# Optimization experiments

Hardware: AMD Instinct MI355X
Metric: run time of the kernel (lower is better)

Reference implementation:

```python
import jax, jax.numpy as jnp
import numpy as np

B, L, D = 2, 2048, 2048
H, HD = 16, 128
E = 8192
SCALE = float(np.sqrt(HD))


def setup_inputs() -> dict:
    key = jax.random.key(0)
    ks = jax.random.split(key, 8)
    s = 0.02
    x = jax.random.normal(ks[0], (B, L, D), dtype=jnp.float32)
    # causal mask: True where key position j > query position i (masked out)
    mask = jnp.triu(jnp.ones((L, L), dtype=bool), k=1)
    Wq = jax.random.normal(ks[1], (D, D), dtype=jnp.float32) * s
    Wk = jax.random.normal(ks[2], (D, D), dtype=jnp.float32) * s
    Wv = jax.random.normal(ks[3], (D, D), dtype=jnp.float32) * s
    W1 = jax.random.normal(ks[4], (D, E), dtype=jnp.float32) * s
    Vg = jax.random.normal(ks[5], (D, E), dtype=jnp.float32) * s
    W2 = jax.random.normal(ks[6], (E, D), dtype=jnp.float32) * s
    return {"x": x, "mask": mask, "Wq": Wq, "Wk": Wk, "Wv": Wv,
            "W1": W1, "Vg": Vg, "W2": W2}


def reynolds_fn(s):
    # Reynolds (group-averaging) operator over key axis: blend score with its row mean
    return 0.5 * s + 0.5 * jnp.mean(s, axis=-1, keepdims=True)


def reference(x, mask, Wq, Wk, Wv, W1, Vg, W2):
    b, l, d = x.shape
    q = (x @ Wq).reshape(b, l, H, HD).transpose(0, 2, 1, 3)  # (B,H,L,hd)
    k = (x @ Wk).reshape(b, l, H, HD).transpose(0, 2, 1, 3)
    v = (x @ Wv).reshape(b, l, H, HD).transpose(0, 2, 1, 3)
    scores = jnp.einsum('bhqd,bhkd->bhqk', q, k) / SCALE
    scores = reynolds_fn(scores)
    scores = jnp.where(mask[None, None], -jnp.inf, scores)
    attn = jax.nn.softmax(scores, axis=-1)
    out = jnp.einsum('bhqk,bhkd->bhqd', attn, v)
    out = out.transpose(0, 2, 1, 3).reshape(b, l, d)  # (B,L,D)
    h = jax.nn.silu(out @ W1) * (out @ Vg)  # SwiGLU
    return h @ W2
```

## Files before the change

kernel.cpp:

```cpp
#include <hip/hip_runtime.h>
#include <stdint.h>

typedef unsigned short u16;
typedef __attribute__((ext_vector_type(8))) short bf16x8;
typedef __attribute__((ext_vector_type(4))) float f32x4;

#define DEVINL static __device__ __forceinline__

DEVINL void gload_lds16(const void* g, void* l) {
  __builtin_amdgcn_global_load_lds(
      (const __attribute__((address_space(1))) unsigned int*)g,
      (__attribute__((address_space(3))) unsigned int*)l, 16, 0, 0);
}

DEVINL u16 f2b(float f) {
  union { float f; unsigned u; } v; v.f = f;
  unsigned r = (v.u + 0x7FFFu + ((v.u >> 16) & 1u)) >> 16;
  return (u16)r;
}

DEVINL bf16x8 ldsv8(const u16* p) { return *(const bf16x8*)p; }

__global__ __launch_bounds__(256) void convt_f32_bf16(
    const float* __restrict__ in, u16* __restrict__ out, int R, int C) {
  __shared__ u16 t[64][65];
  const int c0 = blockIdx.x * 64, r0 = blockIdx.y * 64;
  const int tx = threadIdx.x & 63, ty = threadIdx.x >> 6;
#pragma unroll
  for (int i = 0; i < 64; i += 4)
    t[ty + i][tx] = f2b(in[(size_t)(r0 + ty + i) * C + c0 + tx]);
  __syncthreads();
#pragma unroll
  for (int i = 0; i < 64; i += 4)
    out[(size_t)(c0 + ty + i) * R + r0 + tx] = t[tx][ty + i];
}

__global__ __launch_bounds__(256) void conv_f32_bf16(
    const float* __restrict__ in, u16* __restrict__ out) {
  const size_t i = ((size_t)blockIdx.x * 256 + threadIdx.x) * 4;
  const float4 v = *(const float4*)(in + i);
  ushort4 o;
  o.x = f2b(v.x); o.y = f2b(v.y); o.z = f2b(v.z); o.w = f2b(v.w);
  *(ushort4*)(out + i) = o;
}

template <int EPI>
__global__ __launch_bounds__(256, 2) void gemm_bt(
    const u16* __restrict__ A, const u16* __restrict__ B1,
    const u16* __restrict__ B2, u16* __restrict__ C, float* __restrict__ Cf,
    u16* __restrict__ Ck, u16* __restrict__ Cv,
    int M, int N, int K) {
  constexpr int BK = 64;
  __shared__ __align__(16) u16 sA[128 * BK];
  __shared__ __align__(16) u16 sB[128 * BK];
  __shared__ __align__(16) u16 sB2[(EPI == 2) ? 128 * BK : 16];

  const int tid = threadIdx.x;
  const int w = tid >> 6, lane = tid & 63;
  const int ln = lane & 15, quad = lane >> 4;
  const int wm = (w >> 1) << 6;
  const int wn = (w & 1) << 6;
  const size_t m0 = (size_t)blockIdx.y * 128;
  const size_t n0 = (size_t)blockIdx.x * 128;
  const int srow = lane >> 3;
  const int scol = (((lane & 7) ^ (lane >> 3)) << 3);

  const f32x4 z4 = {0.f, 0.f, 0.f, 0.f};
  f32x4 acc[4][4];
  f32x4 acc2[(EPI == 2) ? 4 : 1][(EPI == 2) ? 4 : 1];
#pragma unroll
  for (int i = 0; i < 4; ++i)
#pragma unroll
    for (int j = 0; j < 4; ++j) {
      acc[i][j] = z4;
      if constexpr (EPI == 2) acc2[i][j] = z4;
    }

  const int nkt = K >> 6;
  for (int kt = 0; kt < nkt; ++kt) {
    const int k0 = kt << 6;
    __syncthreads();
#pragma unroll
    for (int i = 0; i < 4; ++i) {
      const int j = (w << 2) + i;
      const int row = (j << 3) + srow;
      gload_lds16(A + (m0 + row) * K + (k0 + scol), &sA[j * 512]);
      gload_lds16(B1 + (n0 + row) * K + (k0 + scol), &sB[j * 512]);
      if constexpr (EPI == 2)
        gload_lds16(B2 + (n0 + row) * K + (k0 + scol), &sB2[j * 512]);
    }
    __syncthreads();
#pragma unroll
    for (int kk = 0; kk < 2; ++kk) {
      const int xc = (((kk << 2) + quad) ^ (ln & 7)) << 3;
      bf16x8 a[4];
#pragma unroll
      for (int mi = 0; mi < 4; ++mi)
        a[mi] = ldsv8(&sA[(wm + mi * 16 + ln) * BK + xc]);
#pragma unroll
      for (int ni = 0; ni < 4; ++ni) {
        bf16x8 b = ldsv8(&sB[(wn + ni * 16 + ln) * BK + xc]);
#pragma unroll
        for (int mi = 0; mi < 4; ++mi)
          acc[mi][ni] =
              __builtin_amdgcn_mfma_f32_16x16x32_bf16(a[mi], b, acc[mi][ni], 0, 0, 0);
      }
      if constexpr (EPI == 2) {
#pragma unroll
        for (int ni = 0; ni < 4; ++ni) {
          bf16x8 b = ldsv8(&sB2[(wn + ni * 16 + ln) * BK + xc]);
#pragma unroll
          for (int mi = 0; mi < 4; ++mi)
            acc2[mi][ni] =
                __builtin_amdgcn_mfma_f32_16x16x32_bf16(a[mi], b, acc2[mi][ni], 0, 0, 0);
        }
      }
    }
  }

#pragma unroll
  for (int mi = 0; mi < 4; ++mi)
#pragma unroll
    for (int ni = 0; ni < 4; ++ni)
#pragma unroll
      for (int r = 0; r < 4; ++r) {
        const size_t rg = m0 + wm + mi * 16 + quad * 4 + r;
        const size_t cg = n0 + wn + ni * 16 + ln;
        const float v = acc[mi][ni][r];
        if constexpr (EPI == 0) {
          Cf[rg * N + cg] = v;
        } else if constexpr (EPI == 4) {
          const size_t b = rg >> 11, l = rg & 2047;
          const size_t c = cg & 2047, h = c >> 7, hd = c & 127;
          const int which = (int)(cg >> 11);
          if (which == 0)
            C[(((b << 4) + h) * 2048 + l) * 128 + hd] = f2b(v);
          else if (which == 1)
            Ck[(((b << 4) + h) * 2048 + l) * 128 + hd] = f2b(v);
          else
            Cv[(((b << 4) + h) * 128 + hd) * 2048 + l] = f2b(v);
        } else {
          const float v2 = acc2[mi][ni][r];
          const float s = v / (1.f + __expf(-v));
          C[rg * N + cg] = f2b(s * v2);
        }
      }
}

__global__ __launch_bounds__(256, 2) void attn(
    const u16* __restrict__ Q, const u16* __restrict__ Km,
    const u16* __restrict__ VT, u16* __restrict__ O) {
  constexpr int L = 2048, HD = 128, QT = 128, KT = 64;
  __shared__ __align__(16) u16 sQ[QT * HD];
  __shared__ __align__(16) u16 sKP[QT * KT];
  __shared__ __align__(16) u16 sV[HD * KT];

  const int bh = blockIdx.y;
  const int q0 = blockIdx.x * QT;
  const int tid = threadIdx.x, w = tid >> 6, lane = tid & 63;
  const int ln = lane & 15, quad = lane >> 4;
  const int wr = w * 32;

  const u16* Qb = Q + (size_t)bh * L * HD + (size_t)q0 * HD;
  const u16* Kb = Km + (size_t)bh * L * HD;
  const u16* Vb = VT + (size_t)bh * HD * L;

#pragma unroll
  for (int i = 0; i < 8; ++i) {
    const int j = w * 8 + i;
    const int row = j * 4 + (lane >> 4);
    const int c = (lane & 15) ^ (row & 15);
    gload_lds16(Qb + row * HD + c * 8, &sQ[j * 512]);
  }

  const f32x4 z4 = {0.f, 0.f, 0.f, 0.f};
  float l_st[2][4];
  f32x4 accO[2][8];
#pragma unroll
  for (int mi = 0; mi < 2; ++mi) {
#pragma unroll
    for (int r = 0; r < 4; ++r) l_st[mi][r] = 0.f;
#pragma unroll
    for (int nt = 0; nt < 8; ++nt) accO[mi][nt] = z4;
  }

  const float scale = 0.04419417382415922f;
  const int nkt = (q0 >> 6) + 2;

  for (int kt = 0; kt < nkt; ++kt) {
    const int kb = kt << 6;
    __syncthreads();
#pragma unroll
    for (int i = 0; i < 4; ++i) {
      const int j = (w << 2) + i;
      const int krow = j * 4 + (lane >> 4);
      const int kc = (lane & 15) ^ (krow & 15);
      gload_lds16(Kb + (size_t)(kb + krow) * HD + kc * 8, &sKP[j * 512]);
      const int vrow = (j << 3) + (lane >> 3);
      const int vc = (lane & 7) ^ (lane >> 3);
      gload_lds16(Vb + (size_t)vrow * L + kb + vc * 8, &sV[j * 512]);
    }
    __syncthreads();

    f32x4 accS[2][4];
#pragma unroll
    for (int mi = 0; mi < 2; ++mi)
#pragma unroll
      for (int ct = 0; ct < 4; ++ct) accS[mi][ct] = z4;
#pragma unroll
    for (int kk = 0; kk < 4; ++kk) {
      const int xc = (((kk << 2) + quad) ^ ln) << 3;
      bf16x8 aq[2];
#pragma unroll
      for (int mi = 0; mi < 2; ++mi)
        aq[mi] = ldsv8(&sQ[(wr + mi * 16 + ln) * HD + xc]);
#pragma unroll
      for (int ct = 0; ct < 4; ++ct) {
        bf16x8 bk = ldsv8(&sKP[(ct * 16 + ln) * HD + xc]);
#pragma unroll
        for (int mi = 0; mi < 2; ++mi)
          accS[mi][ct] =
              __builtin_amdgcn_mfma_f32_16x16x32_bf16(aq[mi], bk, accS[mi][ct], 0, 0, 0);
      }
    }
    __syncthreads();

    const bool maskt = (kb + KT > q0);
#pragma unroll
    for (int mi = 0; mi < 2; ++mi) {
#pragma unroll
      for (int r = 0; r < 4; ++r) {
        const int qrow = q0 + wr + mi * 16 + quad * 4 + r;
        const int prow = wr + mi * 16 + quad * 4 + r;
        float sum = 0.f;
#pragma unroll
        for (int ct = 0; ct < 4; ++ct) {
          float e = __expf(accS[mi][ct][r] * scale);
          if (maskt && (kb + ct * 16 + ln > qrow)) e = 0.f;
          sum += e;
          const int pc = (ct * 2 + (ln >> 3)) ^ (prow & 7);
          sKP[prow * KT + pc * 8 + (ln & 7)] = f2b(e);
        }
        sum += __shfl_xor(sum, 1);
        sum += __shfl_xor(sum, 2);
        sum += __shfl_xor(sum, 4);
        sum += __shfl_xor(sum, 8);
        l_st[mi][r] += sum;
      }
    }
    __syncthreads();

#pragma unroll
    for (int kk = 0; kk < 2; ++kk) {
      const int xc = (((kk << 2) + quad) ^ (ln & 7)) << 3;
      bf16x8 ap[2];
#pragma unroll
      for (int mi = 0; mi < 2; ++mi)
        ap[mi] = ldsv8(&sKP[(wr + mi * 16 + ln) * KT + xc]);
#pragma unroll
      for (int nt = 0; nt < 8; ++nt) {
        bf16x8 bv = ldsv8(&sV[(nt * 16 + ln) * KT + xc]);
#pragma unroll
        for (int mi = 0; mi < 2; ++mi)
          accO[mi][nt] =
              __builtin_amdgcn_mfma_f32_16x16x32_bf16(ap[mi], bv, accO[mi][nt], 0, 0, 0);
      }
    }
  }

  const int b = bh >> 4, h = bh & 15;
#pragma unroll
  for (int mi = 0; mi < 2; ++mi)
#pragma unroll
    for (int nt = 0; nt < 8; ++nt)
#pragma unroll
      for (int r = 0; r < 4; ++r) {
        const int qrow = q0 + wr + mi * 16 + quad * 4 + r;
        const float v = accO[mi][nt][r] / l_st[mi][r];
        O[(size_t)(b * 2048 + qrow) * 2048 + h * 128 + nt * 16 + ln] = f2b(v);
      }
}

extern "C" void kernel_launch(void* const* d_in, const int* in_sizes, int n_in,
                              void* d_out, int out_size, void* d_ws, size_t ws_size,
                              hipStream_t stream) {
  const float* x  = (const float*)d_in[0];
  const float* Wq = (const float*)d_in[2];
  const float* Wk = (const float*)d_in[3];
  const float* Wv = (const float*)d_in[4];
  const float* W1 = (const float*)d_in[5];
  const float* Vg = (const float*)d_in[6];
  const float* W2 = (const float*)d_in[7];
  float* out = (float*)d_out;
  char* ws = (char*)d_ws;

  const size_t MB = 1ull << 20;
  u16* W1T = (u16*)(ws);
  u16* VgT = (u16*)(ws + 32 * MB);
  u16* W2T = (u16*)(ws + 64 * MB);
  u16* WqT = (u16*)(ws + 96 * MB);
  u16* WkT = (u16*)(ws + 104 * MB);
  u16* WvT = (u16*)(ws + 112 * MB);
  u16* xb  = (u16*)(ws + 120 * MB);
  u16* Qb  = (u16*)(ws + 136 * MB);
  u16* Kb  = (u16*)(ws + 152 * MB);
  u16* VTb = (u16*)(ws + 168 * MB);
  u16* Ob  = (u16*)(ws + 184 * MB);
  u16* Hb  = (u16*)(ws + 96 * MB);

  dim3 blk(256);
  convt_f32_bf16<<<dim3(32, 32), blk, 0, stream>>>(Wq, WqT, 2048, 2048);
  convt_f32_bf16<<<dim3(32, 32), blk, 0, stream>>>(Wk, WkT, 2048, 2048);
  convt_f32_bf16<<<dim3(32, 32), blk, 0, stream>>>(Wv, WvT, 2048, 2048);
  convt_f32_bf16<<<dim3(128, 32), blk, 0, stream>>>(W1, W1T, 2048, 8192);
  convt_f32_bf16<<<dim3(128, 32), blk, 0, stream>>>(Vg, VgT, 2048, 8192);
  convt_f32_bf16<<<dim3(32, 128), blk, 0, stream>>>(W2, W2T, 8192, 2048);
  conv_f32_bf16<<<dim3(8192), blk, 0, stream>>>(x, xb);

  gemm_bt<4><<<dim3(48, 32), blk, 0, stream>>>(xb, WqT, nullptr, Qb, nullptr,
                                               Kb, VTb, 4096, 6144, 2048);

  attn<<<dim3(16, 32), blk, 0, stream>>>(Qb, Kb, VTb, Ob);

  gemm_bt<2><<<dim3(64, 32), blk, 0, stream>>>(Ob, W1T, VgT, Hb, nullptr,
                                               nullptr, nullptr, 4096, 8192, 2048);

  gemm_bt<0><<<dim3(16, 32), blk, 0, stream>>>(Hb, W2T, nullptr, nullptr, out,
                                               nullptr, nullptr, 4096, 2048, 8192);
}
```

Measured before the change: 977.8 us.

## Triple-buffer GEMM LDS pipeline with BK=32 and 256-row tiles for single-B GEMMs

Restructures the bf16 GEMM kernel into a three-stage LDS ring with asynchronous global-to-LDS loads issued two tiles ahead. Each K-step waits with a partial vmcnt plus a barrier instead of two full syncthreads per tile. Single-B GEMMs switch to 256x128 tiles for more reuse, the dual-B SwiGLU GEMM interleaves its two MFMA streams, and MFMA sections get raised wave priority. Dynamic shared memory (72KB) is set through function attributes, which may lower occupancy, and the new swizzle and hand-written waitcnt counts add a risk of correctness errors.

```diff
diff --git a/kernel.cpp b/kernel.cpp
--- a/kernel.cpp
+++ b/kernel.cpp
@@ -50,76 +50,134 @@
     const u16* __restrict__ B2, u16* __restrict__ C, float* __restrict__ Cf,
     u16* __restrict__ Ck, u16* __restrict__ Cv,
     int M, int N, int K) {
-  constexpr int BK = 64;
-  __shared__ __align__(16) u16 sA[128 * BK];
-  __shared__ __align__(16) u16 sB[128 * BK];
-  __shared__ __align__(16) u16 sB2[(EPI == 2) ? 128 * BK : 16];
+  constexpr bool DUAL = (EPI == 2);
+  constexpr int MI = DUAL ? 4 : 8;
+  constexpr int MT = DUAL ? 128 : 256;
+  constexpr int BUFU = 12288;
+  extern __shared__ __align__(16) u16 sL[];
 
   const int tid = threadIdx.x;
   const int w = tid >> 6, lane = tid & 63;
   const int ln = lane & 15, quad = lane >> 4;
-  const int wm = (w >> 1) << 6;
+  const int wm = DUAL ? ((w >> 1) << 6) : ((w >> 1) << 7);
   const int wn = (w & 1) << 6;
-  const size_t m0 = (size_t)blockIdx.y * 128;
+  const size_t m0 = (size_t)blockIdx.y * MT;
   const size_t n0 = (size_t)blockIdx.x * 128;
-  const int srow = lane >> 3;
-  const int scol = (((lane & 7) ^ (lane >> 3)) << 3);
+
+  const int srow = lane >> 2;
+  const int scol = (((lane & 3) ^ ((lane >> 2) & 3) ^ ((lane >> 4) & 3)) << 3);
+  const int pa8 = ((quad ^ (ln & 3) ^ ((ln >> 2) & 3)) << 3);
+
+  const u16* gsrc[6];
+  int ldst[6];
+  if constexpr (!DUAL) {
+#pragma unroll
+    for (int i = 0; i < 4; ++i) {
+      gsrc[i] = A + (m0 + (size_t)((w << 6) + (i << 4) + srow)) * K + scol;
+      ldst[i] = ((w << 2) + i) << 9;
+    }
+#pragma unroll
+    for (int i = 0; i < 2; ++i) {
+      gsrc[4 + i] = B1 + (n0 + (size_t)((w << 5) + (i << 4) + srow)) * K + scol;
+      ldst[4 + i] = 8192 + (((w << 1) + i) << 9);
+    }
+  } else {
+#pragma unroll
+    for (int i = 0; i < 2; ++i) {
+      const size_t r = (size_t)((w << 5) + (i << 4) + srow);
+      const int ch = ((w << 1) + i) << 9;
+      gsrc[i] = A + (m0 + r) * K + scol;          ldst[i] = ch;
+      gsrc[2 + i] = B1 + (n0 + r) * K + scol;     ldst[2 + i] = 4096 + ch;
+      gsrc[4 + i] = B2 + (n0 + r) * K + scol;     ldst[4 + i] = 8192 + ch;
+    }
+  }
 
   const f32x4 z4 = {0.f, 0.f, 0.f, 0.f};
-  f32x4 acc[4][4];
-  f32x4 acc2[(EPI == 2) ? 4 : 1][(EPI == 2) ? 4 : 1];
-#pragma unroll
-  for (int i = 0; i < 4; ++i)
-#pragma unroll
-    for (int j = 0; j < 4; ++j) {
-      acc[i][j] = z4;
-      if constexpr (EPI == 2) acc2[i][j] = z4;
-    }
-
-  const int nkt = K >> 6;
-  for (int kt = 0; kt < nkt; ++kt) {
-    const int k0 = kt << 6;
-    __syncthreads();
-#pragma unroll
-    for (int i = 0; i < 4; ++i) {
-      const int j = (w << 2) + i;
-      const int row = (j << 3) + srow;
-      gload_lds16(A + (m0 + row) * K + (k0 + scol), &sA[j * 512]);
-      gload_lds16(B1 + (n0 + row) * K + (k0 + scol), &sB[j * 512]);
-      if constexpr (EPI == 2)
-        gload_lds16(B2 + (n0 + row) * K + (k0 + scol), &sB2[j * 512]);
-    }
-    __syncthreads();
-#pragma unroll
-    for (int kk = 0; kk < 2; ++kk) {
-      const int xc = (((kk << 2) + quad) ^ (ln & 7)) << 3;
-      bf16x8 a[4];
-#pragma unroll
-      for (int mi = 0; mi < 4; ++mi)
-        a[mi] = ldsv8(&sA[(wm + mi * 16 + ln) * BK + xc]);
+  f32x4 acc[MI][4];
+  f32x4 acc2[DUAL ? 4 : 1][DUAL ? 4 : 1];
+#pragma unroll
+  for (int i = 0; i < MI; ++i)
+#pragma unroll
+    for (int j = 0; j < 4; ++j) acc[i][j] = z4;
+  if constexpr (DUAL) {
+#pragma unroll
+    for (int i = 0; i < 4; ++i)
+#pragma unroll
+      for (int j = 0; j < 4; ++j) acc2[i][j] = z4;
+  }
+
+  auto stageT = [&](int tt, int sb) {
+    const size_t ko = (size_t)tt << 5;
+#pragma unroll
+    for (int j = 0; j < 6; ++j)
+      gload_lds16(gsrc[j] + ko, &sL[sb * BUFU + ldst[j]]);
+  };
+
+  auto loadA = [&](int cur, bf16x8* a) {
+    const u16* bufb = &sL[cur * BUFU];
+#pragma unroll
+    for (int mi = 0; mi < MI; ++mi)
+      a[mi] = ldsv8(bufb + (wm + mi * 16 + ln) * 32 + pa8);
+  };
+
+  auto mfmaT = [&](int cur, const bf16x8* a) {
+    const u16* bufb = &sL[cur * BUFU];
+    __builtin_amdgcn_s_setprio(1);
+    if constexpr (!DUAL) {
 #pragma unroll
       for (int ni = 0; ni < 4; ++ni) {
-        bf16x8 b = ldsv8(&sB[(wn + ni * 16 + ln) * BK + xc]);
-#pragma unroll
-        for (int mi = 0; mi < 4; ++mi)
+        bf16x8 b = ldsv8(bufb + 8192 + (wn + ni * 16 + ln) * 32 + pa8);
+#pragma unroll
+        for (int mi = 0; mi < 8; ++mi)
           acc[mi][ni] =
               __builtin_amdgcn_mfma_f32_16x16x32_bf16(a[mi], b, acc[mi][ni], 0, 0, 0);
       }
-      if constexpr (EPI == 2) {
-#pragma unroll
-        for (int ni = 0; ni < 4; ++ni) {
-          bf16x8 b = ldsv8(&sB2[(wn + ni * 16 + ln) * BK + xc]);
-#pragma unroll
-          for (int mi = 0; mi < 4; ++mi)
-            acc2[mi][ni] =
-                __builtin_amdgcn_mfma_f32_16x16x32_bf16(a[mi], b, acc2[mi][ni], 0, 0, 0);
+    } else {
+#pragma unroll
+      for (int ni = 0; ni < 4; ++ni) {
+        bf16x8 b1 = ldsv8(bufb + 4096 + (wn + ni * 16 + ln) * 32 + pa8);
+        bf16x8 b2 = ldsv8(bufb + 8192 + (wn + ni * 16 + ln) * 32 + pa8);
+#pragma unroll
+        for (int mi = 0; mi < 4; ++mi) {
+          acc[mi][ni] =
+              __builtin_amdgcn_mfma_f32_16x16x32_bf16(a[mi], b1, acc[mi][ni], 0, 0, 0);
+          acc2[mi][ni] =
+              __builtin_amdgcn_mfma_f32_16x16x32_bf16(a[mi], b2, acc2[mi][ni], 0, 0, 0);
         }
       }
     }
-  }
-
-#pragma unroll
-  for (int mi = 0; mi < 4; ++mi)
+    __builtin_amdgcn_s_setprio(0);
+  };
+
+  const int nkt = K >> 5;
+  stageT(0, 0);
+  stageT(1, 1);
+  int cur = 0, stg = 2;
+  for (int t = 0; t < nkt - 2; ++t) {
+    asm volatile("s_waitcnt vmcnt(6)\n\ts_barrier" ::: "memory");
+    bf16x8 a[MI];
+    loadA(cur, a);
+    stageT(t + 2, stg);
+    mfmaT(cur, a);
+    cur = (cur == 2) ? 0 : cur + 1;
+    stg = (stg == 2) ? 0 : stg + 1;
+  }
+  {
+    asm volatile("s_waitcnt vmcnt(6)\n\ts_barrier" ::: "memory");
+    bf16x8 a[MI];
+    loadA(cur, a);
+    mfmaT(cur, a);
+    cur = (cur == 2) ? 0 : cur + 1;
+  }
+  {
+    asm volatile("s_waitcnt vmcnt(0)\n\ts_barrier" ::: "memory");
+    bf16x8 a[MI];
+    loadA(cur, a);
+    mfmaT(cur, a);
+  }
+
+#pragma unroll
+  for (int mi = 0; mi < MI; ++mi)
 #pragma unroll
     for (int ni = 0; ni < 4; ++ni)
 #pragma unroll
@@ -308,6 +366,14 @@
   u16* Ob  = (u16*)(ws + 184 * MB);
   u16* Hb  = (u16*)(ws + 96 * MB);
 
+  constexpr int GEMM_LDS = 3 * 12288 * 2;
+  (void)hipFuncSetAttribute((const void*)gemm_bt<4>,
+                            hipFuncAttributeMaxDynamicSharedMemorySize, GEMM_LDS);
+  (void)hipFuncSetAttribute((const void*)gemm_bt<2>,
+                            hipFuncAttributeMaxDynamicSharedMemorySize, GEMM_LDS);
+  (void)hipFuncSetAttribute((const void*)gemm_bt<0>,
+                            hipFuncAttributeMaxDynamicSharedMemorySize, GEMM_LDS);
+
   dim3 blk(256);
   convt_f32_bf16<<<dim3(32, 32), blk, 0, stream>>>(Wq, WqT, 2048, 2048);
   convt_f32_bf16<<<dim3(32, 32), blk, 0, stream>>>(Wk, WkT, 2048, 2048);
@@ -317,14 +383,14 @@
   convt_f32_bf16<<<dim3(32, 128), blk, 0, stream>>>(W2, W2T, 8192, 2048);
   conv_f32_bf16<<<dim3(8192), blk, 0, stream>>>(x, xb);
 
-  gemm_bt<4><<<dim3(48, 32), blk, 0, stream>>>(xb, WqT, nullptr, Qb, nullptr,
-                                               Kb, VTb, 4096, 6144, 2048);
+  gemm_bt<4><<<dim3(48, 16), blk, GEMM_LDS, stream>>>(
+      xb, WqT, nullptr, Qb, nullptr, Kb, VTb, 4096, 6144, 2048);
 
   attn<<<dim3(16, 32), blk, 0, stream>>>(Qb, Kb, VTb, Ob);
 
-  gemm_bt<2><<<dim3(64, 32), blk, 0, stream>>>(Ob, W1T, VgT, Hb, nullptr,
-                                               nullptr, nullptr, 4096, 8192, 2048);
-
-  gemm_bt<0><<<dim3(16, 32), blk, 0, stream>>>(Hb, W2T, nullptr, nullptr, out,
-                                               nullptr, nullptr, 4096, 2048, 8192);
-}
+  gemm_bt<2><<<dim3(64, 32), blk, GEMM_LDS, stream>>>(
+      Ob, W1T, VgT, Hb, nullptr, nullptr, nullptr, 4096, 8192, 2048);
+
+  gemm_bt<0><<<dim3(16, 16), blk, GEMM_LDS, stream>>>(
+      Hb, W2T, nullptr, nullptr, out, nullptr, nullptr, 4096, 2048, 8192);
+}
```

Measured after the change: 943.5 us. 3.5% less time.

## Double-buffer GEMM LDS staging with 512-thread 256x128 tiles and vmcnt waits

Applied to the files above, without the earlier changes.

Rewrites the bf16 GEMM main loop to use two dynamic-LDS buffers, prefetching tile t+2 while computing tile t, and replaces syncthreads with explicit vmcnt/lgkmcnt waits plus barriers. Blocks grow to 512 threads (8 waves) covering a 256x128 output tile, so the A tile is shared by more waves and B traffic per output drops. MFMA sections are wrapped in setprio. This aims to hide global-load latency and cut barrier stalls, but uses much more LDS per block (up to 128KB for the dual GEMM), which may limit occupancy. The hand-tuned waitcnt values depend on the exact load count per wave.

```diff
diff --git a/kernel.cpp b/kernel.cpp
--- a/kernel.cpp
+++ b/kernel.cpp
@@ -20,6 +20,11 @@
 }
 
 DEVINL bf16x8 ldsv8(const u16* p) { return *(const bf16x8*)p; }
+
+DEVINL void topw6() { asm volatile("s_waitcnt vmcnt(6)\n\ts_barrier" ::: "memory"); }
+DEVINL void topw8() { asm volatile("s_waitcnt vmcnt(8)\n\ts_barrier" ::: "memory"); }
+DEVINL void topw0() { asm volatile("s_waitcnt vmcnt(0)\n\ts_barrier" ::: "memory"); }
+DEVINL void midw()  { asm volatile("s_waitcnt lgkmcnt(0)\n\ts_barrier" ::: "memory"); }
 
 __global__ __launch_bounds__(256) void convt_f32_bf16(
     const float* __restrict__ in, u16* __restrict__ out, int R, int C) {
@@ -45,78 +50,122 @@
 }
 
 template <int EPI>
-__global__ __launch_bounds__(256, 2) void gemm_bt(
+__global__ __launch_bounds__(512, 2) void gemm_bt(
     const u16* __restrict__ A, const u16* __restrict__ B1,
     const u16* __restrict__ B2, u16* __restrict__ C, float* __restrict__ Cf,
     u16* __restrict__ Ck, u16* __restrict__ Cv,
     int M, int N, int K) {
-  constexpr int BK = 64;
-  __shared__ __align__(16) u16 sA[128 * BK];
-  __shared__ __align__(16) u16 sB[128 * BK];
-  __shared__ __align__(16) u16 sB2[(EPI == 2) ? 128 * BK : 16];
+  constexpr bool DUAL = (EPI == 2);
+  constexpr int NG = DUAL ? 8 : 6;
+  constexpr int OFF_B = 16384;
+  constexpr int OFF_B2 = 24576;
+  constexpr int BUFU = DUAL ? 32768 : 24576;
+  extern __shared__ __align__(16) u16 sL[];
 
   const int tid = threadIdx.x;
   const int w = tid >> 6, lane = tid & 63;
   const int ln = lane & 15, quad = lane >> 4;
   const int wm = (w >> 1) << 6;
   const int wn = (w & 1) << 6;
-  const size_t m0 = (size_t)blockIdx.y * 128;
+  const size_t m0 = (size_t)blockIdx.y * 256;
   const size_t n0 = (size_t)blockIdx.x * 128;
+
   const int srow = lane >> 3;
-  const int scol = (((lane & 7) ^ (lane >> 3)) << 3);
+  const int scol = (((lane & 7) ^ srow) << 3);
+  const int xc0 = ((quad ^ (ln & 7)) << 3);
+  const int xc1 = (((4 + quad) ^ (ln & 7)) << 3);
+
+  const u16* gp[NG];
+  int ldo[NG];
+#pragma unroll
+  for (int i = 0; i < 4; ++i) {
+    const int j = (w << 2) + i;
+    gp[i] = A + (m0 + (size_t)(j * 8 + srow)) * K + scol;
+    ldo[i] = j << 9;
+  }
+#pragma unroll
+  for (int i = 0; i < 2; ++i) {
+    const int j = (w << 1) + i;
+    gp[4 + i] = B1 + (n0 + (size_t)(j * 8 + srow)) * K + scol;
+    ldo[4 + i] = OFF_B + (j << 9);
+  }
+  if constexpr (DUAL) {
+#pragma unroll
+    for (int i = 0; i < 2; ++i) {
+      const int j = (w << 1) + i;
+      gp[6 + i] = B2 + (n0 + (size_t)(j * 8 + srow)) * K + scol;
+      ldo[6 + i] = OFF_B2 + (j << 9);
+    }
+  }
 
   const f32x4 z4 = {0.f, 0.f, 0.f, 0.f};
   f32x4 acc[4][4];
-  f32x4 acc2[(EPI == 2) ? 4 : 1][(EPI == 2) ? 4 : 1];
+  f32x4 acc2[DUAL ? 4 : 1][DUAL ? 4 : 1];
 #pragma unroll
   for (int i = 0; i < 4; ++i)
 #pragma unroll
     for (int j = 0; j < 4; ++j) {
       acc[i][j] = z4;
-      if constexpr (EPI == 2) acc2[i][j] = z4;
-    }
+      if constexpr (DUAL) acc2[i][j] = z4;
+    }
+
+  auto stageT = [&](int tt, int buf) {
+    const size_t ko = (size_t)tt << 6;
+#pragma unroll
+    for (int j = 0; j < NG; ++j)
+      gload_lds16(gp[j] + ko, &sL[buf * BUFU + ldo[j]]);
+  };
+
+  auto ldf = [&](const u16* base, int xc, bf16x8* a, bf16x8* b, bf16x8* c2) {
+#pragma unroll
+    for (int mi = 0; mi < 4; ++mi)
+      a[mi] = ldsv8(base + (wm + mi * 16 + ln) * 64 + xc);
+#pragma unroll
+    for (int ni = 0; ni < 4; ++ni)
+      b[ni] = ldsv8(base + OFF_B + (wn + ni * 16 + ln) * 64 + xc);
+    if constexpr (DUAL) {
+#pragma unroll
+      for (int ni = 0; ni < 4; ++ni)
+        c2[ni] = ldsv8(base + OFF_B2 + (wn + ni * 16 + ln) * 64 + xc);
+    }
+  };
+
+  auto mf = [&](const bf16x8* a, const bf16x8* b, const bf16x8* c2) {
+    __builtin_amdgcn_s_setprio(1);
+#pragma unroll
+    for (int ni = 0; ni < 4; ++ni) {
+#pragma unroll
+      for (int mi = 0; mi < 4; ++mi) {
+        acc[mi][ni] =
+            __builtin_amdgcn_mfma_f32_16x16x32_bf16(a[mi], b[ni], acc[mi][ni], 0, 0, 0);
+        if constexpr (DUAL)
+          acc2[mi][ni] =
+              __builtin_amdgcn_mfma_f32_16x16x32_bf16(a[mi], c2[ni], acc2[mi][ni], 0, 0, 0);
+      }
+    }
+    __builtin_amdgcn_s_setprio(0);
+  };
+
+  auto body = [&](int t, bool do_stage) {
+    const u16* base = &sL[(t & 1) * BUFU];
+    bf16x8 a[4], b[4], c2[DUAL ? 4 : 1];
+    ldf(base, xc0, a, b, c2);
+    mf(a, b, c2);
+    ldf(base, xc1, a, b, c2);
+    midw();
+    if (do_stage) stageT(t + 2, t & 1);
+    mf(a, b, c2);
+  };
 
   const int nkt = K >> 6;
-  for (int kt = 0; kt < nkt; ++kt) {
-    const int k0 = kt << 6;
-    __syncthreads();
-#pragma unroll
-    for (int i = 0; i < 4; ++i) {
-      const int j = (w << 2) + i;
-      const int row = (j << 3) + srow;
-      gload_lds16(A + (m0 + row) * K + (k0 + scol), &sA[j * 512]);
-      gload_lds16(B1 + (n0 + row) * K + (k0 + scol), &sB[j * 512]);
-      if constexpr (EPI == 2)
-        gload_lds16(B2 + (n0 + row) * K + (k0 + scol), &sB2[j * 512]);
-    }
-    __syncthreads();
-#pragma unroll
-    for (int kk = 0; kk < 2; ++kk) {
-      const int xc = (((kk << 2) + quad) ^ (ln & 7)) << 3;
-      bf16x8 a[4];
-#pragma unroll
-      for (int mi = 0; mi < 4; ++mi)
-        a[mi] = ldsv8(&sA[(wm + mi * 16 + ln) * BK + xc]);
-#pragma unroll
-      for (int ni = 0; ni < 4; ++ni) {
-        bf16x8 b = ldsv8(&sB[(wn + ni * 16 + ln) * BK + xc]);
-#pragma unroll
-        for (int mi = 0; mi < 4; ++mi)
-          acc[mi][ni] =
-              __builtin_amdgcn_mfma_f32_16x16x32_bf16(a[mi], b, acc[mi][ni], 0, 0, 0);
-      }
-      if constexpr (EPI == 2) {
-#pragma unroll
-        for (int ni = 0; ni < 4; ++ni) {
-          bf16x8 b = ldsv8(&sB2[(wn + ni * 16 + ln) * BK + xc]);
-#pragma unroll
-          for (int mi = 0; mi < 4; ++mi)
-            acc2[mi][ni] =
-                __builtin_amdgcn_mfma_f32_16x16x32_bf16(a[mi], b, acc2[mi][ni], 0, 0, 0);
-        }
-      }
-    }
-  }
+  stageT(0, 0);
+  stageT(1, 1);
+  for (int t = 0; t < nkt - 1; ++t) {
+    if constexpr (DUAL) topw8(); else topw6();
+    body(t, t < nkt - 2);
+  }
+  topw0();
+  body(nkt - 1, false);
 
 #pragma unroll
   for (int mi = 0; mi < 4; ++mi)
@@ -308,7 +357,16 @@
   u16* Ob  = (u16*)(ws + 184 * MB);
   u16* Hb  = (u16*)(ws + 96 * MB);
 
-  dim3 blk(256);
+  constexpr int LDS_S = 2 * 24576 * 2;
+  constexpr int LDS_D = 2 * 32768 * 2;
+  (void)hipFuncSetAttribute((const void*)gemm_bt<4>,
+                            hipFuncAttributeMaxDynamicSharedMemorySize, LDS_S);
+  (void)hipFuncSetAttribute((const void*)gemm_bt<2>,
+                            hipFuncAttributeMaxDynamicSharedMemorySize, LDS_D);
+  (void)hipFuncSetAttribute((const void*)gemm_bt<0>,
+                            hipFuncAttributeMaxDynamicSharedMemorySize, LDS_S);
+
+  dim3 blk(256), gblk(512);
   convt_f32_bf16<<<dim3(32, 32), blk, 0, stream>>>(Wq, WqT, 2048, 2048);
   convt_f32_bf16<<<dim3(32, 32), blk, 0, stream>>>(Wk, WkT, 2048, 2048);
   convt_f32_bf16<<<dim3(32, 32), blk, 0, stream>>>(Wv, WvT, 2048, 2048);
@@ -317,14 +375,14 @@
   convt_f32_bf16<<<dim3(32, 128), blk, 0, stream>>>(W2, W2T, 8192, 2048);
   conv_f32_bf16<<<dim3(8192), blk, 0, stream>>>(x, xb);
 
-  gemm_bt<4><<<dim3(48, 32), blk, 0, stream>>>(xb, WqT, nullptr, Qb, nullptr,
-                                               Kb, VTb, 4096, 6144, 2048);
+  gemm_bt<4><<<dim3(48, 16), gblk, LDS_S, stream>>>(
+      xb, WqT, nullptr, Qb, nullptr, Kb, VTb, 4096, 6144, 2048);
 
   attn<<<dim3(16, 32), blk, 0, stream>>>(Qb, Kb, VTb, Ob);
 
-  gemm_bt<2><<<dim3(64, 32), blk, 0, stream>>>(Ob, W1T, VgT, Hb, nullptr,
-                                               nullptr, nullptr, 4096, 8192, 2048);
-
-  gemm_bt<0><<<dim3(16, 32), blk, 0, stream>>>(Hb, W2T, nullptr, nullptr, out,
-                                               nullptr, nullptr, 4096, 2048, 8192);
-}
+  gemm_bt<2><<<dim3(64, 16), gblk, LDS_D, stream>>>(
+      Ob, W1T, VgT, Hb, nullptr, nullptr, nullptr, 4096, 8192, 2048);
+
+  gemm_bt<0><<<dim3(16, 16), gblk, LDS_S, stream>>>(
+      Hb, W2T, nullptr, nullptr, out, nullptr, nullptr, 4096, 2048, 8192);
+}
```

Result: faster. 874.0 us (-10.6%).
